# Performance work log

Measured on AMD Instinct MI355X. Metric: run time of the kernel, lower is better.

The kernel has to match this reference:

```python
import jax, jax.numpy as jnp
import numpy as np

NUM_CLASSES = 4
GAMMA = 2.0          # FocalLoss gamma
T_ALPHA, T_BETA = 0.3, 0.7
SMOOTH = 1e-5
W_DICE, W_CE, W_BOUND = 1.0, 1.0, 0.01
INF = 1e12


def _dt1d(f):
    # min-plus 1D squared distance transform along last axis (brute Felzenszwalb)
    n = f.shape[-1]
    i = jnp.arange(n, dtype=f.dtype)
    d2 = (i[:, None] - i[None, :]) ** 2          # [n, n]
    return jnp.min(f[..., None, :] + d2, axis=-1)


def _edt(seed):
    # Euclidean distance from every voxel to the nearest True voxel in `seed`
    f = jnp.where(seed, 0.0, INF).astype(jnp.float32)
    for ax in range(f.ndim):
        f = jnp.moveaxis(_dt1d(jnp.moveaxis(f, ax, -1)), -1, ax)
    return jnp.sqrt(f)


def _sdf(mask):
    # signed distance map, matching compute_edt_map (mask: bool [D,H,W])
    s = mask.sum()
    size = mask.size
    dist_out = _edt(mask)        # scipy distance(1-mask)
    dist_in = _edt(~mask)        # scipy distance(mask)
    sdf = dist_out - dist_in
    sdf = jnp.where(s == 0, 1.0, jnp.where(s == size, -1.0, sdf))
    return sdf


def setup_inputs() -> dict:
    key = jax.random.key(0)
    k1, k2 = jax.random.split(key)
    preds = jax.random.normal(k1, (4, NUM_CLASSES, 64, 64, 64), dtype=jnp.float32)
    targets = jax.random.randint(k2, (4, 64, 64, 64), 0, NUM_CLASSES).astype(jnp.int64)
    return {"preds": preds, "targets": targets}


def reference(preds, targets):
    B = preds.shape[0]
    sp_dims = (2, 3, 4)

    probs = jax.nn.softmax(preds, axis=1)                       # [B,C,D,H,W]
    onehot = (targets[:, None] == jnp.arange(NUM_CLASSES)[None, :, None, None, None]).astype(preds.dtype)

    # ---- Tversky ----
    TP = jnp.sum(probs * onehot, axis=sp_dims)
    FP = jnp.sum(probs * (1.0 - onehot), axis=sp_dims)
    FN = jnp.sum((1.0 - probs) * onehot, axis=sp_dims)
    tversky = (TP + SMOOTH) / (TP + T_ALPHA * FP + T_BETA * FN + SMOOTH)
    l_dice = 1.0 - tversky.mean()

    # ---- Focal ----
    logp = jax.nn.log_softmax(preds, axis=1)
    ce = -jnp.take_along_axis(logp, targets[:, None], axis=1)[:, 0]   # [B,D,H,W]
    pt = jnp.exp(-ce)
    l_main = jnp.mean((1.0 - pt) ** GAMMA * ce)

    # ---- Boundary ----
    masks = targets[:, None] == jnp.arange(1, NUM_CLASSES)[None, :, None, None, None]  # [B,3,D,H,W] bool
    flat = masks.reshape((-1,) + masks.shape[2:])
    sdfs = jax.lax.map(_sdf, flat).reshape(masks.shape)               # [B,3,D,H,W]
    nonempty = jnp.sum(masks, axis=sp_dims) > 0                       # [B,3]
    contrib = jnp.mean(sdfs * probs[:, 1:NUM_CLASSES], axis=sp_dims)  # [B,3]
    l_bound = jnp.sum(jnp.where(nonempty, contrib, 0.0)) / (B * (NUM_CLASSES - 1) + 1e-8)

    return W_DICE * l_dice + W_CE * l_main + W_BOUND * l_bound
```

## Files before the change

kernel.cpp:

```cpp
#include <hip/hip_runtime.h>
#include <math.h>

#define SPATIAL 262144
#define NVOX    1048576
#define NVOL    12
#define FAR_D2  50000
#define NPART   13
#define RCHUNK  256

typedef unsigned short u16x2 __attribute__((ext_vector_type(2)));
union pku { unsigned int u; u16x2 v; };

__device__ __forceinline__ unsigned int pk_min(unsigned int a, unsigned int b) {
    pku x, y; x.u = a; y.u = b;
    x.v = __builtin_elementwise_min(x.v, y.v);
    return x.u;
}
__device__ __forceinline__ unsigned int pk_max(unsigned int a, unsigned int b) {
    pku x, y; x.u = a; y.u = b;
    x.v = __builtin_elementwise_max(x.v, y.v);
    return x.u;
}


__device__ __forceinline__ void voxel_accum(float p0, float p1, float p2, float p3,
                                            int t, float* loc) {
    float m = fmaxf(fmaxf(p0, p1), fmaxf(p2, p3));
    float e0 = __expf(p0 - m), e1 = __expf(p1 - m);
    float e2 = __expf(p2 - m), e3 = __expf(p3 - m);
    float s = e0 + e1 + e2 + e3;
    float inv = __builtin_amdgcn_rcpf(s);
    float q0 = e0 * inv, q1 = e1 * inv, q2 = e2 * inv, q3 = e3 * inv;
    float pl = (t == 0) ? p0 : (t == 1) ? p1 : (t == 2) ? p2 : p3;
    float ce = __logf(s) + (m - pl);
    float qt = (t == 0) ? q0 : (t == 1) ? q1 : (t == 2) ? q2 : q3;
    float om = 1.0f - qt;
    loc[0] += q0; loc[1] += q1; loc[2] += q2; loc[3] += q3;
    if (t == 0)      { loc[4] += q0; loc[8]  += 1.f; }
    else if (t == 1) { loc[5] += q1; loc[9]  += 1.f; }
    else if (t == 2) { loc[6] += q2; loc[10] += 1.f; }
    else             { loc[7] += q3; loc[11] += 1.f; }
    loc[12] += om * om * ce;
}

__global__ __launch_bounds__(256) void reduce_kernel(
        const float* __restrict__ preds, const int* __restrict__ targets,
        float* __restrict__ partials) {
    int bb = blockIdx.x;
    int b = bb >> 8, chunk = bb & 255;
    int tid = threadIdx.x;
    const float* pb = preds + (size_t)b * 4 * SPATIAL;
    const int* tb = targets + b * SPATIAL;
    float loc[NPART];
    #pragma unroll
    for (int k = 0; k < NPART; ++k) loc[k] = 0.0f;

    int sp = chunk * 1024 + tid * 4;
    float4 P0 = *(const float4*)(pb + 0 * SPATIAL + sp);
    float4 P1 = *(const float4*)(pb + 1 * SPATIAL + sp);
    float4 P2 = *(const float4*)(pb + 2 * SPATIAL + sp);
    float4 P3 = *(const float4*)(pb + 3 * SPATIAL + sp);
    int4   T  = *(const int4*)(tb + sp);
    voxel_accum(P0.x, P1.x, P2.x, P3.x, T.x, loc);
    voxel_accum(P0.y, P1.y, P2.y, P3.y, T.y, loc);
    voxel_accum(P0.z, P1.z, P2.z, P3.z, T.z, loc);
    voxel_accum(P0.w, P1.w, P2.w, P3.w, T.w, loc);

    int lane = tid & 63, w = tid >> 6;
    #pragma unroll
    for (int k = 0; k < NPART; ++k) {
        float v = loc[k];
        #pragma unroll
        for (int off = 32; off > 0; off >>= 1)
            v += __shfl_down(v, off, 64);
        loc[k] = v;
    }
    __shared__ float sred[NPART][4];
    if (lane == 0) {
        #pragma unroll
        for (int k = 0; k < NPART; ++k) sred[k][w] = loc[k];
    }
    __syncthreads();
    if (tid < NPART) {
        float tot = sred[tid][0] + sred[tid][1] + sred[tid][2] + sred[tid][3];
        partials[(b * NPART + tid) * RCHUNK + chunk] = tot;
    }
}


__device__ __forceinline__ int row_d2i(unsigned long long m, int i) {
    if (m == 0ull) return FAR_D2;
    unsigned long long right = m >> i;
    unsigned long long left  = m << (63 - i);
    int dr = right ? __builtin_ctzll(right) : 1000;
    int dl = left  ? __builtin_clzll(left)  : 1000;
    int d = (dr < dl) ? dr : dl;
    return d * d;
}

#define MINPLUS_PK(LA, ACC, LANE, W)                                            \
    {                                                                           \
        const int base = (W) * 8;                                               \
        _Pragma("unroll")                                                       \
        for (int jj = 0; jj < 8; ++jj) {                                        \
            unsigned int wv = LA[(base + jj) * 64 + (LANE)];                    \
            _Pragma("unroll")                                                   \
            for (int k = 0; k < 8; ++k) {                                       \
                int d = k - jj;                                                 \
                unsigned int dd = (unsigned int)(d * d);                        \
                ACC[k] = pk_min(ACC[k], wv + (dd | (dd << 16)));                \
            }                                                                   \
        }                                                                       \
        const int el_max = base, er_max = 56 - base;                            \
        int t = 1;                                                              \
        while (true) {                                                          \
            unsigned int am = 0;                                                \
            _Pragma("unroll")                                                   \
            for (int k = 0; k < 8; ++k) am = pk_max(am, ACC[k]);                \
            _Pragma("unroll")                                                   \
            for (int off = 32; off > 0; off >>= 1)                              \
                am = pk_max(am, (unsigned int)__shfl_xor((int)am, off, 64));    \
            int amx = (int)(am & 0xFFFFu), amy = (int)(am >> 16);               \
            int mm = (amx > amy) ? amx : amy;                                   \
            int dmax = (int)sqrtf((float)mm) + 1;     \
            int Tl = (dmax < el_max) ? dmax : el_max;                           \
            int Tr = (dmax < er_max) ? dmax : er_max;                           \
            int T = (Tl > Tr) ? Tl : Tr;                                        \
            if (t > T) break;                                                   \
            int tend = (T < t + 3) ? T : (t + 3);                               \
            for (; t <= tend; ++t) {                                            \
                if (t <= Tl) {                                                  \
                    unsigned int wv = LA[(base - t) * 64 + (LANE)];             \
                    _Pragma("unroll")                                           \
                    for (int k = 0; k < 8; ++k) {                               \
                        int d = t + k;                                          \
                        unsigned int dd = (unsigned int)(d * d);                \
                        ACC[k] = pk_min(ACC[k], wv + (dd | (dd << 16)));        \
                    }                                                           \
                }                                                               \
                if (t <= Tr) {                                                  \
                    unsigned int wv = LA[(base + 7 + t) * 64 + (LANE)];         \
                    _Pragma("unroll")                                           \
                    for (int k = 0; k < 8; ++k) {                               \
                        int d = t + 7 - k;                                      \
                        unsigned int dd = (unsigned int)(d * d);                \
                        ACC[k] = pk_min(ACC[k], wv + (dd | (dd << 16)));        \
                    }                                                           \
                }                                                               \
            }                                                                   \
        }                                                                       \
    }

__global__ __launch_bounds__(512) void dtxy_kernel(
        const int* __restrict__ targets, unsigned int* __restrict__ dtp) {
    __shared__ unsigned int la[4096];
    int blk = blockIdx.x;
    int v = blk >> 6, z = blk & 63;
    int b = v / 3, cls = (v % 3) + 1;
    const int* tp = targets + b * SPATIAL + z * 4096;
    int t = threadIdx.x, lane = t & 63, w = t >> 6;

    #pragma unroll
    for (int k = 0; k < 8; ++k) {
        int y = w * 8 + k;
        int tv = tp[y * 64 + lane];
        unsigned long long m = __ballot(tv == cls);
        int do2 = row_d2i(m, lane);
        int di2 = row_d2i(~m, lane);
        la[y * 64 + lane] = (unsigned int)do2 | ((unsigned int)di2 << 16);
    }
    __syncthreads();

    unsigned int acc[8];
    #pragma unroll
    for (int k = 0; k < 8; ++k) acc[k] = 0xFFFFFFFFu;
    MINPLUS_PK(la, acc, lane, w)

    size_t vol = (size_t)v * SPATIAL;
    #pragma unroll
    for (int k = 0; k < 8; ++k) {
        int i = w * 8 + k;
        dtp[vol + (size_t)z * 4096 + (size_t)i * 64 + lane] = acc[k];
    }
}

__global__ __launch_bounds__(512) void dtz_final_kernel(
        const unsigned int* __restrict__ dtp, const float* __restrict__ preds,
        float* __restrict__ bound) {
    __shared__ unsigned int la[4096];
    int blk = blockIdx.x;
    int v = blk >> 6, y = blk & 63;
    int b = v / 3, cls = (v % 3) + 1;
    size_t vol = (size_t)v * SPATIAL;
    int t = threadIdx.x, lane = t & 63, w = t >> 6;

    #pragma unroll
    for (int k = 0; k < 8; ++k) {
        int idx = k * 512 + t;
        int zz = idx >> 6, x = idx & 63;
        la[idx] = dtp[vol + (size_t)zz * 4096 + (size_t)y * 64 + x];
    }
    __syncthreads();

    unsigned int acc[8];
    #pragma unroll
    for (int k = 0; k < 8; ++k) acc[k] = 0xFFFFFFFFu;
    MINPLUS_PK(la, acc, lane, w)

    float partial = 0.0f;
    const float* pbase = preds + (size_t)b * 4 * SPATIAL;
    #pragma unroll
    for (int k = 0; k < 8; ++k) {
        int i = w * 8 + k;
        size_t sp = (size_t)i * 4096 + (size_t)y * 64 + lane;
        float dout = (float)(acc[k] & 0xFFFFu);
        float din  = (float)(acc[k] >> 16);
        float sv = sqrtf(dout) - sqrtf(din);
        float p0 = pbase[sp], p1 = pbase[SPATIAL + sp];
        float p2 = pbase[2 * SPATIAL + sp], p3 = pbase[3 * SPATIAL + sp];
        float m = fmaxf(fmaxf(p0, p1), fmaxf(p2, p3));
        float e0 = __expf(p0 - m), e1 = __expf(p1 - m);
        float e2 = __expf(p2 - m), e3 = __expf(p3 - m);
        float s = e0 + e1 + e2 + e3;
        float ec = (cls == 1) ? e1 : (cls == 2) ? e2 : e3;
        partial += sv * (ec * __builtin_amdgcn_rcpf(s));
    }
    #pragma unroll
    for (int off = 32; off > 0; off >>= 1)
        partial += __shfl_down(partial, off, 64);
    __shared__ float ws8[8];
    if (lane == 0) ws8[w] = partial;
    __syncthreads();
    if (t == 0) {
        float tot = 0.0f;
        #pragma unroll
        for (int i = 0; i < 8; ++i) tot += ws8[i];
        bound[blk] = tot;
    }
}

__global__ __launch_bounds__(256) void final_kernel(
        const float* __restrict__ partials, const float* __restrict__ bound,
        float* __restrict__ out) {
    __shared__ float rowsum[52];
    __shared__ float bsum[12];
    int tid = threadIdx.x, lane = tid & 63, w = tid >> 6;

    for (int r = w; r < 52; r += 4) {
        const float* p = partials + r * RCHUNK;
        float v = p[lane] + p[64 + lane] + p[128 + lane] + p[192 + lane];
        #pragma unroll
        for (int off = 32; off > 0; off >>= 1)
            v += __shfl_down(v, off, 64);
        if (lane == 0) rowsum[r] = v;
    }
    for (int r = w; r < 12; r += 4) {
        float v = bound[r * 64 + lane];
        #pragma unroll
        for (int off = 32; off > 0; off >>= 1)
            v += __shfl_down(v, off, 64);
        if (lane == 0) bsum[r] = v;
    }
    __syncthreads();
    if (tid != 0) return;

    float tsum = 0.0f;
    for (int b = 0; b < 4; ++b)
        for (int c = 0; c < 4; ++c) {
            float S  = rowsum[b * NPART + c];
            float TP = rowsum[b * NPART + 4 + c];
            float CN = rowsum[b * NPART + 8 + c];
            float FP = S - TP;
            float FN = CN - TP;
            tsum += (TP + 1e-5f) / (TP + 0.3f * FP + 0.7f * FN + 1e-5f);
        }
    float l_dice = 1.0f - tsum / 16.0f;
    float l_main = (rowsum[12] + rowsum[NPART + 12] +
                    rowsum[2 * NPART + 12] + rowsum[3 * NPART + 12]) / (float)NVOX;
    float bs = 0.0f;
    for (int v = 0; v < NVOL; ++v) {
        int b = v / 3, c = (v % 3) + 1;
        float CN = rowsum[b * NPART + 8 + c];
        float contrib;
        if (CN <= 0.0f) contrib = 0.0f;
        else if (CN >= (float)SPATIAL) contrib = -rowsum[b * NPART + c] / (float)SPATIAL;
        else contrib = bsum[v] / (float)SPATIAL;
        bs += contrib;
    }
    float l_bound = bs / (12.0f + 1e-8f);
    out[0] = l_dice + l_main + 0.01f * l_bound;
}

extern "C" void kernel_launch(void* const* d_in, const int* in_sizes, int n_in,
                              void* d_out, int out_size, void* d_ws, size_t ws_size,
                              hipStream_t stream) {
    const float* preds = (const float*)d_in[0];
    const int* targets = (const int*)d_in[1];
    float* out = (float*)d_out;
    float* ws = (float*)d_ws;
    float* partials = ws;
    float* bound = ws + 4 * NPART * RCHUNK;
    unsigned int* dtp = (unsigned int*)(ws + 4 * NPART * RCHUNK + NVOL * 64);

    hipLaunchKernelGGL(reduce_kernel, dim3(4 * RCHUNK), dim3(256), 0, stream,
                       preds, targets, partials);
    hipLaunchKernelGGL(dtxy_kernel, dim3(NVOL * 64), dim3(512), 0, stream,
                       targets, dtp);
    hipLaunchKernelGGL(dtz_final_kernel, dim3(NVOL * 64), dim3(512), 0, stream,
                       dtp, preds, bound);
    hipLaunchKernelGGL(final_kernel, dim3(1), dim3(256), 0, stream,
                       partials, bound, out);
}
```

Before: 110.7 us.

## Fuse Tversky/focal reduction into z-distance kernel and widen min-plus batch

Removes the separate reduce kernel and computes the softmax/Tversky/focal partial sums inside the z-pass distance kernel, in the blocks for class 1. Those blocks already load all four class logits for each voxel, so only the target load is added. This saves one full pass over preds and one launch, but adds register pressure and uneven work across the class-1 blocks. It also raises the min-plus inner batch from 4 to 8 steps between convergence checks, which means fewer reductions but possibly wasted iterations.

```diff
diff --git a/kernel.cpp b/kernel.cpp
--- a/kernel.cpp
+++ b/kernel.cpp
@@ -6,7 +6,6 @@
 #define NVOL    12
 #define FAR_D2  50000
 #define NPART   13
-#define RCHUNK  256
 
 typedef unsigned short u16x2 __attribute__((ext_vector_type(2)));
 union pku { unsigned int u; u16x2 v; };
@@ -21,72 +20,6 @@
     x.v = __builtin_elementwise_max(x.v, y.v);
     return x.u;
 }
-
-
-__device__ __forceinline__ void voxel_accum(float p0, float p1, float p2, float p3,
-                                            int t, float* loc) {
-    float m = fmaxf(fmaxf(p0, p1), fmaxf(p2, p3));
-    float e0 = __expf(p0 - m), e1 = __expf(p1 - m);
-    float e2 = __expf(p2 - m), e3 = __expf(p3 - m);
-    float s = e0 + e1 + e2 + e3;
-    float inv = __builtin_amdgcn_rcpf(s);
-    float q0 = e0 * inv, q1 = e1 * inv, q2 = e2 * inv, q3 = e3 * inv;
-    float pl = (t == 0) ? p0 : (t == 1) ? p1 : (t == 2) ? p2 : p3;
-    float ce = __logf(s) + (m - pl);
-    float qt = (t == 0) ? q0 : (t == 1) ? q1 : (t == 2) ? q2 : q3;
-    float om = 1.0f - qt;
-    loc[0] += q0; loc[1] += q1; loc[2] += q2; loc[3] += q3;
-    if (t == 0)      { loc[4] += q0; loc[8]  += 1.f; }
-    else if (t == 1) { loc[5] += q1; loc[9]  += 1.f; }
-    else if (t == 2) { loc[6] += q2; loc[10] += 1.f; }
-    else             { loc[7] += q3; loc[11] += 1.f; }
-    loc[12] += om * om * ce;
-}
-
-__global__ __launch_bounds__(256) void reduce_kernel(
-        const float* __restrict__ preds, const int* __restrict__ targets,
-        float* __restrict__ partials) {
-    int bb = blockIdx.x;
-    int b = bb >> 8, chunk = bb & 255;
-    int tid = threadIdx.x;
-    const float* pb = preds + (size_t)b * 4 * SPATIAL;
-    const int* tb = targets + b * SPATIAL;
-    float loc[NPART];
-    #pragma unroll
-    for (int k = 0; k < NPART; ++k) loc[k] = 0.0f;
-
-    int sp = chunk * 1024 + tid * 4;
-    float4 P0 = *(const float4*)(pb + 0 * SPATIAL + sp);
-    float4 P1 = *(const float4*)(pb + 1 * SPATIAL + sp);
-    float4 P2 = *(const float4*)(pb + 2 * SPATIAL + sp);
-    float4 P3 = *(const float4*)(pb + 3 * SPATIAL + sp);
-    int4   T  = *(const int4*)(tb + sp);
-    voxel_accum(P0.x, P1.x, P2.x, P3.x, T.x, loc);
-    voxel_accum(P0.y, P1.y, P2.y, P3.y, T.y, loc);
-    voxel_accum(P0.z, P1.z, P2.z, P3.z, T.z, loc);
-    voxel_accum(P0.w, P1.w, P2.w, P3.w, T.w, loc);
-
-    int lane = tid & 63, w = tid >> 6;
-    #pragma unroll
-    for (int k = 0; k < NPART; ++k) {
-        float v = loc[k];
-        #pragma unroll
-        for (int off = 32; off > 0; off >>= 1)
-            v += __shfl_down(v, off, 64);
-        loc[k] = v;
-    }
-    __shared__ float sred[NPART][4];
-    if (lane == 0) {
-        #pragma unroll
-        for (int k = 0; k < NPART; ++k) sred[k][w] = loc[k];
-    }
-    __syncthreads();
-    if (tid < NPART) {
-        float tot = sred[tid][0] + sred[tid][1] + sred[tid][2] + sred[tid][3];
-        partials[(b * NPART + tid) * RCHUNK + chunk] = tot;
-    }
-}
-
 
 __device__ __forceinline__ int row_d2i(unsigned long long m, int i) {
     if (m == 0ull) return FAR_D2;
@@ -127,7 +60,7 @@
             int Tr = (dmax < er_max) ? dmax : er_max;                           \
             int T = (Tl > Tr) ? Tl : Tr;                                        \
             if (t > T) break;                                                   \
-            int tend = (T < t + 3) ? T : (t + 3);                               \
+            int tend = (T < t + 7) ? T : (t + 7);                               \
             for (; t <= tend; ++t) {                                            \
                 if (t <= Tl) {                                                  \
                     unsigned int wv = LA[(base - t) * 64 + (LANE)];             \
@@ -184,9 +117,10 @@
     }
 }
 
-__global__ __launch_bounds__(512) void dtz_final_kernel(
+__global__ __launch_bounds__(512) void dtz_fused_kernel(
         const unsigned int* __restrict__ dtp, const float* __restrict__ preds,
-        float* __restrict__ bound) {
+        const int* __restrict__ targets,
+        float* __restrict__ bound, float* __restrict__ rpart) {
     __shared__ unsigned int la[4096];
     int blk = blockIdx.x;
     int v = blk >> 6, y = blk & 63;
@@ -207,8 +141,14 @@
     for (int k = 0; k < 8; ++k) acc[k] = 0xFFFFFFFFu;
     MINPLUS_PK(la, acc, lane, w)
 
+    const bool doRed = (cls == 1);
+    float loc[NPART];
+    #pragma unroll
+    for (int k = 0; k < NPART; ++k) loc[k] = 0.0f;
+
     float partial = 0.0f;
     const float* pbase = preds + (size_t)b * 4 * SPATIAL;
+    const int* tbase = targets + b * SPATIAL;
     #pragma unroll
     for (int k = 0; k < 8; ++k) {
         int i = w * 8 + k;
@@ -222,15 +162,55 @@
         float e0 = __expf(p0 - m), e1 = __expf(p1 - m);
         float e2 = __expf(p2 - m), e3 = __expf(p3 - m);
         float s = e0 + e1 + e2 + e3;
+        float inv = __builtin_amdgcn_rcpf(s);
         float ec = (cls == 1) ? e1 : (cls == 2) ? e2 : e3;
-        partial += sv * (ec * __builtin_amdgcn_rcpf(s));
-    }
+        partial += sv * (ec * inv);
+        if (doRed) {
+            int tv = tbase[sp];
+            float q0 = e0 * inv, q1 = e1 * inv, q2 = e2 * inv, q3 = e3 * inv;
+            float pl = (tv == 0) ? p0 : (tv == 1) ? p1 : (tv == 2) ? p2 : p3;
+            float ce = __logf(s) + (m - pl);
+            float qt = (tv == 0) ? q0 : (tv == 1) ? q1 : (tv == 2) ? q2 : q3;
+            float om = 1.0f - qt;
+            loc[0] += q0; loc[1] += q1; loc[2] += q2; loc[3] += q3;
+            if (tv == 0)      { loc[4] += q0; loc[8]  += 1.f; }
+            else if (tv == 1) { loc[5] += q1; loc[9]  += 1.f; }
+            else if (tv == 2) { loc[6] += q2; loc[10] += 1.f; }
+            else              { loc[7] += q3; loc[11] += 1.f; }
+            loc[12] += om * om * ce;
+        }
+    }
+
     #pragma unroll
     for (int off = 32; off > 0; off >>= 1)
         partial += __shfl_down(partial, off, 64);
     __shared__ float ws8[8];
     if (lane == 0) ws8[w] = partial;
-    __syncthreads();
+
+    if (doRed) {
+        __shared__ float sred[NPART][8];
+        #pragma unroll
+        for (int k = 0; k < NPART; ++k) {
+            float vv = loc[k];
+            #pragma unroll
+            for (int off = 32; off > 0; off >>= 1)
+                vv += __shfl_down(vv, off, 64);
+            loc[k] = vv;
+        }
+        if (lane == 0) {
+            #pragma unroll
+            for (int k = 0; k < NPART; ++k) sred[k][w] = loc[k];
+        }
+        __syncthreads();
+        if (t < NPART) {
+            float tot = 0.0f;
+            #pragma unroll
+            for (int i = 0; i < 8; ++i) tot += sred[t][i];
+            rpart[(b * NPART + t) * 64 + y] = tot;
+        }
+    } else {
+        __syncthreads();
+    }
     if (t == 0) {
         float tot = 0.0f;
         #pragma unroll
@@ -240,15 +220,14 @@
 }
 
 __global__ __launch_bounds__(256) void final_kernel(
-        const float* __restrict__ partials, const float* __restrict__ bound,
+        const float* __restrict__ rpart, const float* __restrict__ bound,
         float* __restrict__ out) {
     __shared__ float rowsum[52];
     __shared__ float bsum[12];
     int tid = threadIdx.x, lane = tid & 63, w = tid >> 6;
 
     for (int r = w; r < 52; r += 4) {
-        const float* p = partials + r * RCHUNK;
-        float v = p[lane] + p[64 + lane] + p[128 + lane] + p[192 + lane];
+        float v = rpart[r * 64 + lane];
         #pragma unroll
         for (int off = 32; off > 0; off >>= 1)
             v += __shfl_down(v, off, 64);
@@ -298,16 +277,14 @@
     const int* targets = (const int*)d_in[1];
     float* out = (float*)d_out;
     float* ws = (float*)d_ws;
-    float* partials = ws;
-    float* bound = ws + 4 * NPART * RCHUNK;
-    unsigned int* dtp = (unsigned int*)(ws + 4 * NPART * RCHUNK + NVOL * 64);
-
-    hipLaunchKernelGGL(reduce_kernel, dim3(4 * RCHUNK), dim3(256), 0, stream,
-                       preds, targets, partials);
+    float* rpart = ws;
+    float* bound = ws + 4 * NPART * 64;
+    unsigned int* dtp = (unsigned int*)(ws + 4 * NPART * 64 + NVOL * 64);
+
     hipLaunchKernelGGL(dtxy_kernel, dim3(NVOL * 64), dim3(512), 0, stream,
                        targets, dtp);
-    hipLaunchKernelGGL(dtz_final_kernel, dim3(NVOL * 64), dim3(512), 0, stream,
-                       dtp, preds, bound);
+    hipLaunchKernelGGL(dtz_fused_kernel, dim3(NVOL * 64), dim3(512), 0, stream,
+                       dtp, preds, targets, bound, rpart);
     hipLaunchKernelGGL(final_kernel, dim3(1), dim3(256), 0, stream,
-                       partials, bound, out);
-}
+                       rpart, bound, out);
+}
```

New measurement: 104.0 us. -6.1%, faster.
